# Kernel tuning notes

Hardware: AMD Instinct MI355X
Metric: run time of the kernel (lower is better)

Reference implementation:

```python
import jax, jax.numpy as jnp
import numpy as np

B, L, D, Y = 8, 2500, 512, 8921


def setup_inputs() -> dict:
    key = jax.random.key(0)
    k1, k2, k3, k4, k5 = jax.random.split(key, 5)
    x = jax.random.normal(k1, (B, L, D), dtype=jnp.float32)
    target = jax.random.uniform(k2, (B, Y), dtype=jnp.float32)
    U_w = jax.random.normal(k3, (Y, D), dtype=jnp.float32) * (1.0 / np.sqrt(D))
    final_w = jax.random.normal(k4, (Y, D), dtype=jnp.float32) * (1.0 / np.sqrt(D))
    final_b = jax.random.normal(k5, (Y,), dtype=jnp.float32) * 0.01
    return {"x": x, "target": target, "text_inputs": 0,
            "U_w": U_w, "final_w": final_w, "final_b": final_b}


def _bce_with_logits(y, t):
    # stable mean BCE-with-logits, matching torch BCEWithLogitsLoss (reduction='mean')
    return jnp.mean(jnp.maximum(y, 0.0) - y * t + jnp.log1p(jnp.exp(-jnp.abs(y))))


def reference(x, target, text_inputs, U_w, final_w, final_b):
    # label-wise attention scores: [B, Y, L]
    scores = jnp.einsum('yd,bld->byl', U_w, x)
    alpha = jax.nn.softmax(scores, axis=-1)
    # attended context per label: [B, Y, D]
    m = jnp.einsum('byl,bld->byd', alpha, x)
    # per-label dot-product readout: [B, Y]
    y = jnp.einsum('yd,byd->by', final_w, m) + final_b
    loss = _bce_with_logits(y, target)
    return (y, loss)
```

## Files before the change

kernel.cpp:

```cpp
#include <hip/hip_runtime.h>
#include <math.h>

#define B_  8
#define L_  2500
#define D_  512
#define Y_  8921
#define LP  2560
#define YP  8960

#define WS_F16_HALVES  (B_ * LP * D_ + 2 * YP * D_)
#define ACC_FLOATS     (2 * B_ * YP)

typedef _Float16 f16x8 __attribute__((ext_vector_type(8)));
typedef float    f32x4 __attribute__((ext_vector_type(4)));

__device__ __forceinline__ void load_lds16(const _Float16* g, _Float16* l) {
  __builtin_amdgcn_global_load_lds(
      (const __attribute__((address_space(1))) unsigned int*)g,
      (__attribute__((address_space(3))) unsigned int*)l, 16, 0, 0);
}

__global__ void k_convert(const float* __restrict__ x,
                          const float* __restrict__ Uw,
                          const float* __restrict__ Fw,
                          _Float16* __restrict__ ws,
                          float* __restrict__ loss_slot) {
  if (blockIdx.x == 0 && threadIdx.x == 0) *loss_slot = 0.0f;
  const int NX = B_ * LP * (D_ / 8);
  const int NU = YP * (D_ / 8);
  int idx = blockIdx.x * 256 + threadIdx.x;
  if (idx < ACC_FLOATS) ((float*)(ws + WS_F16_HALVES))[idx] = 0.0f;
  const float* src = nullptr;
  if (idx < NX) {
    int b  = idx / (LP * 64);
    int r  = idx - b * (LP * 64);
    int l  = r >> 6;
    int d8 = r & 63;
    if (l < L_) src = x + (((long)b * L_ + l) * D_ + d8 * 8);
  } else if (idx < NX + NU) {
    int u = idx - NX;
    int y = u >> 6, d8 = u & 63;
    if (y < Y_) src = Uw + ((long)y * D_ + d8 * 8);
  } else {
    int u = idx - NX - NU;
    int y = u >> 6, d8 = u & 63;
    if (y < Y_) src = Fw + ((long)y * D_ + d8 * 8);
  }
  f16x8 o;
  if (src) {
    const float4* s4 = (const float4*)src;
    float4 a = s4[0], c = s4[1];
    o[0] = (_Float16)a.x; o[1] = (_Float16)a.y; o[2] = (_Float16)a.z; o[3] = (_Float16)a.w;
    o[4] = (_Float16)c.x; o[5] = (_Float16)c.y; o[6] = (_Float16)c.z; o[7] = (_Float16)c.w;
  } else {
    for (int i = 0; i < 8; ++i) o[i] = (_Float16)0.0f;
  }
  ((f16x8*)ws)[idx] = o;
}

__global__ __launch_bounds__(512, 2)
void k_attn(const _Float16* __restrict__ ws,
            float* __restrict__ accG) {
  __shared__ __align__(16) _Float16 TILE[32768];

  const int tid  = threadIdx.x;
  const int lane = tid & 63;
  const int wave = tid >> 6;
  const int wy = wave & 1, wl = wave >> 1;
  const int yt = blockIdx.x;
  const int b  = blockIdx.y;
  const int lh = blockIdx.z;

  const _Float16* Xg = ws + (long)b * LP * D_ + (long)lh * (LP / 2) * D_;
  const _Float16* Ug = ws + (long)B_ * LP * D_ + (long)yt * 128 * D_;
  const _Float16* Fg = Ug + (long)YP * D_;

  const int srow = lane >> 3;
  const int sg8  = ((lane & 7) ^ srow) * 8;

  const int arow = wy * 64 + (lane & 15);
  const int xrow = wl * 64 + (lane & 15);
  const int r7   = lane & 7;
  const int gb   = lane >> 4;

  _Float16* UT = TILE;
  _Float16* FT = TILE + 8192;
  _Float16* XT = TILE + 16384;

  float denP[4][4], numP[4][4];
  for (int i = 0; i < 4; ++i)
    for (int v = 0; v < 4; ++v) { denP[i][v] = 0.0f; numP[i][v] = 0.0f; }

  for (int lt = 0; lt < 5; ++lt) {
    f32x4 Sacc[4][4], Cacc[4][4];
    for (int mi = 0; mi < 4; ++mi)
      for (int ni = 0; ni < 4; ++ni) {
        f32x4 z = {0.0f, 0.0f, 0.0f, 0.0f};
        Sacc[mi][ni] = z; Cacc[mi][ni] = z;
      }
    const _Float16* Xt = Xg + (long)lt * 256 * D_;
    for (int kk = 0; kk < D_; kk += 64) {
      __syncthreads();
      for (int i = 0; i < 8; ++i) {
        int seg = wave * 8 + i;
        const _Float16* g;
        if (seg < 16)      g = Ug + (long)(seg * 8 + srow) * D_;
        else if (seg < 32) g = Fg + (long)((seg - 16) * 8 + srow) * D_;
        else               g = Xt + (long)((seg - 32) * 8 + srow) * D_;
        load_lds16(g + kk + sg8, TILE + seg * 512);
      }
      __syncthreads();
      for (int ks = 0; ks < 2; ++ks) {
        int off = (((ks * 4 + gb) ^ r7) * 8);
        f16x8 au[4], af[4], bx[4];
        for (int mi = 0; mi < 4; ++mi) au[mi] = *(const f16x8*)&UT[(arow + mi * 16) * 64 + off];
        for (int mi = 0; mi < 4; ++mi) af[mi] = *(const f16x8*)&FT[(arow + mi * 16) * 64 + off];
        for (int ni = 0; ni < 4; ++ni) bx[ni] = *(const f16x8*)&XT[(xrow + ni * 16) * 64 + off];
        for (int mi = 0; mi < 4; ++mi)
          for (int ni = 0; ni < 4; ++ni) {
            Sacc[mi][ni] = __builtin_amdgcn_mfma_f32_16x16x32_f16(au[mi], bx[ni], Sacc[mi][ni], 0, 0, 0);
            Cacc[mi][ni] = __builtin_amdgcn_mfma_f32_16x16x32_f16(af[mi], bx[ni], Cacc[mi][ni], 0, 0, 0);
          }
      }
    }
    for (int ni = 0; ni < 4; ++ni)
      for (int mi = 0; mi < 4; ++mi)
        for (int v = 0; v < 4; ++v) {
          float e = __expf(Sacc[mi][ni][v]);
          denP[mi][v] += e;
          numP[mi][v] += e * Cacc[mi][ni][v];
        }
  }

  for (int m = 1; m < 16; m <<= 1)
    for (int mi = 0; mi < 4; ++mi)
      for (int v = 0; v < 4; ++v) {
        denP[mi][v] += __shfl_xor(denP[mi][v], m, 64);
        numP[mi][v] += __shfl_xor(numP[mi][v], m, 64);
      }
  if ((lane & 15) == 0) {
    float* denG = accG;
    float* numG = accG + B_ * YP;
    for (int mi = 0; mi < 4; ++mi)
      for (int v = 0; v < 4; ++v) {
        int y = yt * 128 + wy * 64 + mi * 16 + gb * 4 + v;
        atomicAdd(&denG[b * YP + y], denP[mi][v]);
        atomicAdd(&numG[b * YP + y], numP[mi][v]);
      }
  }
}

__global__ void k_final(const float* __restrict__ accG,
                        const float* __restrict__ fb,
                        float* __restrict__ out) {
  int id = blockIdx.x * 256 + threadIdx.x;
  if (id >= B_ * Y_) return;
  int b = id / Y_, y = id - b * Y_;
  const float* denG = accG;
  const float* numG = accG + B_ * YP;
  float den = denG[b * YP + y] - (float)(LP - L_);
  out[id] = numG[b * YP + y] / den + fb[y];
}

__global__ void k_loss(const float* __restrict__ y,
                       const float* __restrict__ t,
                       float* __restrict__ loss) {
  float p = 0.0f;
  for (int i = blockIdx.x * 256 + threadIdx.x; i < B_ * Y_; i += gridDim.x * 256) {
    float v = y[i], tg = t[i];
    p += fmaxf(v, 0.0f) - v * tg + log1pf(__expf(-fabsf(v)));
  }
  for (int m = 32; m; m >>= 1) p += __shfl_down(p, m, 64);
  __shared__ float wsum[4];
  int lane = threadIdx.x & 63, wv = threadIdx.x >> 6;
  if (lane == 0) wsum[wv] = p;
  __syncthreads();
  if (threadIdx.x == 0) {
    float s = wsum[0] + wsum[1] + wsum[2] + wsum[3];
    atomicAdd(loss, s * (1.0f / (float)(B_ * Y_)));
  }
}

extern "C" void kernel_launch(void* const* d_in, const int* in_sizes, int n_in,
                              void* d_out, int out_size, void* d_ws, size_t ws_size,
                              hipStream_t stream) {
  (void)in_sizes; (void)n_in; (void)out_size; (void)ws_size;
  const float* x       = (const float*)d_in[0];
  const float* target  = (const float*)d_in[1];
  const float* U_w     = (const float*)d_in[3];
  const float* final_w = (const float*)d_in[4];
  const float* final_b = (const float*)d_in[5];
  float* out = (float*)d_out;
  _Float16* ws = (_Float16*)d_ws;
  float* accG = (float*)(ws + WS_F16_HALVES);

  k_convert<<<9600, 256, 0, stream>>>(x, U_w, final_w, ws, out + B_ * Y_);

  dim3 g(YP / 128, B_, 2);
  k_attn<<<g, 512, 0, stream>>>(ws, accG);

  k_final<<<(B_ * Y_ + 255) / 256, 256, 0, stream>>>(accG, final_b, out);
  k_loss<<<140, 256, 0, stream>>>(out, target, out + B_ * Y_);
}
```

Baseline: 592.0 us.

## Split score and readout GEMMs across wave groups, exchanging exp via LDS

The attention kernel previously had each wave compute both the U·x score tile and the F·x readout tile, holding two accumulator sets. Now the waves split into two groups: one computes scores, takes exp and writes fp16 exp values to shared memory, and the other computes the readout tile and multiplies it by those exp values. This halves accumulator registers per wave, shrinks the L tile to 128 and LDS to 48KB, and raises the occupancy target to 4 blocks per CU. In exchange it adds extra barriers, an LDS round trip of exp values rounded to fp16, and twice as many L tiles.

```diff
diff --git a/kernel.cpp b/kernel.cpp
--- a/kernel.cpp
+++ b/kernel.cpp
@@ -12,6 +12,7 @@
 #define ACC_FLOATS     (2 * B_ * YP)
 
 typedef _Float16 f16x8 __attribute__((ext_vector_type(8)));
+typedef _Float16 f16x4 __attribute__((ext_vector_type(4)));
 typedef float    f32x4 __attribute__((ext_vector_type(4)));
 
 __device__ __forceinline__ void load_lds16(const _Float16* g, _Float16* l) {
@@ -58,15 +59,21 @@
   ((f16x8*)ws)[idx] = o;
 }
 
-__global__ __launch_bounds__(512, 2)
+__global__ __launch_bounds__(512, 4)
 void k_attn(const _Float16* __restrict__ ws,
             float* __restrict__ accG) {
-  __shared__ __align__(16) _Float16 TILE[32768];
+  __shared__ __align__(16) _Float16 TILE[24576];
+  _Float16* UT = TILE;
+  _Float16* FT = TILE + 8192;
+  _Float16* XT = TILE + 16384;
+  _Float16* E  = TILE;
 
   const int tid  = threadIdx.x;
   const int lane = tid & 63;
   const int wave = tid >> 6;
-  const int wy = wave & 1, wl = wave >> 1;
+  const int g  = wave & 1;
+  const int wy = (wave >> 1) & 1;
+  const int wl = wave >> 2;
   const int yt = blockIdx.x;
   const int b  = blockIdx.y;
   const int lh = blockIdx.z;
@@ -77,75 +84,113 @@
 
   const int srow = lane >> 3;
   const int sg8  = ((lane & 7) ^ srow) * 8;
+  const _Float16* gsrc[6];
+  _Float16*       gdst[6];
+  #pragma unroll
+  for (int i = 0; i < 6; ++i) {
+    int seg = wave * 6 + i;
+    const _Float16* base;
+    int r;
+    if (seg < 16)      { base = Ug; r = seg * 8; }
+    else if (seg < 32) { base = Fg; r = (seg - 16) * 8; }
+    else               { base = Xg; r = (seg - 32) * 8; }
+    gsrc[i] = base + (long)(r + srow) * D_ + sg8;
+    gdst[i] = TILE + seg * 512;
+  }
 
   const int arow = wy * 64 + (lane & 15);
   const int xrow = wl * 64 + (lane & 15);
   const int r7   = lane & 7;
   const int gb   = lane >> 4;
-
-  _Float16* UT = TILE;
-  _Float16* FT = TILE + 8192;
-  _Float16* XT = TILE + 16384;
-
-  float denP[4][4], numP[4][4];
+  const int c    = lane & 15;
+  const _Float16* AT = g ? FT : UT;
+
+  float redP[4][4];
   for (int i = 0; i < 4; ++i)
-    for (int v = 0; v < 4; ++v) { denP[i][v] = 0.0f; numP[i][v] = 0.0f; }
-
-  for (int lt = 0; lt < 5; ++lt) {
-    f32x4 Sacc[4][4], Cacc[4][4];
+    for (int v = 0; v < 4; ++v) redP[i][v] = 0.0f;
+
+  for (int lt = 0; lt < 10; ++lt) {
+    f32x4 acc[4][4];
+    #pragma unroll
     for (int mi = 0; mi < 4; ++mi)
       for (int ni = 0; ni < 4; ++ni) {
         f32x4 z = {0.0f, 0.0f, 0.0f, 0.0f};
-        Sacc[mi][ni] = z; Cacc[mi][ni] = z;
-      }
-    const _Float16* Xt = Xg + (long)lt * 256 * D_;
+        acc[mi][ni] = z;
+      }
+    const long xofs = (long)lt * 128 * D_;
     for (int kk = 0; kk < D_; kk += 64) {
       __syncthreads();
-      for (int i = 0; i < 8; ++i) {
-        int seg = wave * 8 + i;
-        const _Float16* g;
-        if (seg < 16)      g = Ug + (long)(seg * 8 + srow) * D_;
-        else if (seg < 32) g = Fg + (long)((seg - 16) * 8 + srow) * D_;
-        else               g = Xt + (long)((seg - 32) * 8 + srow) * D_;
-        load_lds16(g + kk + sg8, TILE + seg * 512);
+      #pragma unroll
+      for (int i = 0; i < 6; ++i) {
+        const _Float16* s = gsrc[i] + kk;
+        if (wave * 6 + i >= 32) s += xofs;
+        load_lds16(s, gdst[i]);
       }
       __syncthreads();
+      #pragma unroll
       for (int ks = 0; ks < 2; ++ks) {
         int off = (((ks * 4 + gb) ^ r7) * 8);
-        f16x8 au[4], af[4], bx[4];
-        for (int mi = 0; mi < 4; ++mi) au[mi] = *(const f16x8*)&UT[(arow + mi * 16) * 64 + off];
-        for (int mi = 0; mi < 4; ++mi) af[mi] = *(const f16x8*)&FT[(arow + mi * 16) * 64 + off];
-        for (int ni = 0; ni < 4; ++ni) bx[ni] = *(const f16x8*)&XT[(xrow + ni * 16) * 64 + off];
-        for (int mi = 0; mi < 4; ++mi)
-          for (int ni = 0; ni < 4; ++ni) {
-            Sacc[mi][ni] = __builtin_amdgcn_mfma_f32_16x16x32_f16(au[mi], bx[ni], Sacc[mi][ni], 0, 0, 0);
-            Cacc[mi][ni] = __builtin_amdgcn_mfma_f32_16x16x32_f16(af[mi], bx[ni], Cacc[mi][ni], 0, 0, 0);
+        f16x8 bx[4];
+        #pragma unroll
+        for (int ni = 0; ni < 4; ++ni)
+          bx[ni] = *(const f16x8*)&XT[(xrow + ni * 16) * 64 + off];
+        #pragma unroll
+        for (int mi = 0; mi < 4; ++mi) {
+          f16x8 a = *(const f16x8*)&AT[(arow + mi * 16) * 64 + off];
+          #pragma unroll
+          for (int ni = 0; ni < 4; ++ni)
+            acc[mi][ni] = __builtin_amdgcn_mfma_f32_16x16x32_f16(a, bx[ni], acc[mi][ni], 0, 0, 0);
+        }
+      }
+    }
+    __syncthreads();
+    if (g == 0) {
+      #pragma unroll
+      for (int mi = 0; mi < 4; ++mi) {
+        int yg = wy * 16 + mi * 4 + gb;
+        #pragma unroll
+        for (int ni = 0; ni < 4; ++ni) {
+          f16x4 ev;
+          #pragma unroll
+          for (int v = 0; v < 4; ++v) {
+            float e = __expf(acc[mi][ni][v]);
+            redP[mi][v] += e;
+            ev[v] = (_Float16)e;
           }
+          int l = wl * 64 + ni * 16 + c;
+          *(f16x4*)&E[l * 128 + ((yg ^ c) << 2)] = ev;
+        }
       }
     }
-    for (int ni = 0; ni < 4; ++ni)
-      for (int mi = 0; mi < 4; ++mi)
-        for (int v = 0; v < 4; ++v) {
-          float e = __expf(Sacc[mi][ni][v]);
-          denP[mi][v] += e;
-          numP[mi][v] += e * Cacc[mi][ni][v];
+    __syncthreads();
+    if (g == 1) {
+      #pragma unroll
+      for (int mi = 0; mi < 4; ++mi) {
+        int yg = wy * 16 + mi * 4 + gb;
+        #pragma unroll
+        for (int ni = 0; ni < 4; ++ni) {
+          int l = wl * 64 + ni * 16 + c;
+          f16x4 ev = *(const f16x4*)&E[l * 128 + ((yg ^ c) << 2)];
+          #pragma unroll
+          for (int v = 0; v < 4; ++v)
+            redP[mi][v] += (float)ev[v] * acc[mi][ni][v];
         }
+      }
+    }
   }
 
   for (int m = 1; m < 16; m <<= 1)
+    #pragma unroll
     for (int mi = 0; mi < 4; ++mi)
-      for (int v = 0; v < 4; ++v) {
-        denP[mi][v] += __shfl_xor(denP[mi][v], m, 64);
-        numP[mi][v] += __shfl_xor(numP[mi][v], m, 64);
-      }
+      for (int v = 0; v < 4; ++v)
+        redP[mi][v] += __shfl_xor(redP[mi][v], m, 64);
   if ((lane & 15) == 0) {
-    float* denG = accG;
-    float* numG = accG + B_ * YP;
+    float* dst = accG + (g ? B_ * YP : 0);
+    #pragma unroll
     for (int mi = 0; mi < 4; ++mi)
       for (int v = 0; v < 4; ++v) {
         int y = yt * 128 + wy * 64 + mi * 16 + gb * 4 + v;
-        atomicAdd(&denG[b * YP + y], denP[mi][v]);
-        atomicAdd(&numG[b * YP + y], numP[mi][v]);
+        atomicAdd(&dst[b * YP + y], redP[mi][v]);
       }
   }
 }
@@ -156,10 +201,8 @@
   int id = blockIdx.x * 256 + threadIdx.x;
   if (id >= B_ * Y_) return;
   int b = id / Y_, y = id - b * Y_;
-  const float* denG = accG;
-  const float* numG = accG + B_ * YP;
-  float den = denG[b * YP + y] - (float)(LP - L_);
-  out[id] = numG[b * YP + y] / den + fb[y];
+  float den = accG[b * YP + y] - (float)(LP - L_);
+  out[id] = accG[B_ * YP + b * YP + y] / den + fb[y];
 }
 
 __global__ void k_loss(const float* __restrict__ y,
```

Result: slower. 659.7 us (+11.4%).
